# Kernel tuning notes

Hardware: AMD Instinct MI355X
Metric: run time of the kernel (lower is better)

The kernel has to match this reference:

```python
import jax, jax.numpy as jnp
import numpy as np

EPS = 1e-6
NH = 8     # num_head
WIN = 7    # window

def _ln(x, w, b):
    # channels_last LayerNorm over the final dim
    m = x.mean(-1, keepdims=True)
    v = ((x - m) ** 2).mean(-1, keepdims=True)
    return (x - m) / jnp.sqrt(v + EPS) * w + b

def _dwconv7(x, w, b):
    # x: (B, C, H, W); w: (C, 1, 7, 7) depthwise kernel; padding 3 (SAME for k=7)
    y = jax.lax.conv_general_dilated(
        x, w, window_strides=(1, 1), padding=((3, 3), (3, 3)),
        feature_group_count=x.shape[1],
        dimension_numbers=('NCHW', 'OIHW', 'NCHW'))
    return y + b[None, :, None, None]

def _forward(x, x_e, ln_w, ln_b, lne_w, lne_b, q_w, q_b, qcut_w, qcut_b,
             a_w, a_b, l_w, l_b, conv_w, conv_b, econv_w, econv_b,
             efore_w, efore_b, eback_w, eback_b, kv_w, kv_b,
             scl_w, scl_b, proj_w, proj_b, proje_w, proje_b):
    B, H, W, C = x.shape
    hd = C // NH // 2  # attention head dim (kv is split into k and v halves)

    xn = _ln(x, ln_w, ln_b)          # (B,H,W,C)
    xen = _ln(x_e, lne_w, lne_b)     # (B,H,W,C//2)

    # global shortcut branch (window != 0)
    short = jnp.concatenate([xn, xen], axis=3).transpose(0, 3, 1, 2)  # (B, 3C/2, H, W)

    q = xn @ q_w + q_b                # (B,H,W,C)
    cut = xn @ qcut_w + qcut_b        # (B,H,W,C//2)

    xl = jax.nn.gelu(xn @ l_w + l_b, approximate=False).transpose(0, 3, 1, 2)  # (B,C,H,W)
    a = _dwconv7(xl, conv_w, conv_b).transpose(0, 2, 3, 1) @ a_w + a_b          # (B,H,W,C)

    # kv from the activated l-branch (pre-conv)
    bfeat = xl.transpose(0, 2, 3, 1)                                  # (B,H,W,C)
    kv = (bfeat @ kv_w + kv_b).reshape(B, H * W, 2, NH, hd).transpose(2, 0, 3, 1, 4)
    k, v = kv[0], kv[1]                                               # (B,NH,HW,hd)

    # AdaptiveAvgPool2d((7,7)); H,W divisible by 7 -> exact uniform block mean
    pooled = short.reshape(B, -1, WIN, H // WIN, WIN, W // WIN).mean(axis=(3, 5))  # (B,3C/2,7,7)
    pooled = pooled.transpose(0, 2, 3, 1) @ scl_w + scl_b             # (B,7,7,C//2)
    m = pooled.reshape(B, WIN * WIN, NH, hd).transpose(0, 2, 1, 3)    # (B,NH,49,hd)

    attn = jax.nn.softmax((m * hd ** -0.5) @ jnp.swapaxes(k, -2, -1), axis=-1)  # (B,NH,49,HW)
    ao = (attn @ v).reshape(B, NH, WIN, WIN, hd).transpose(0, 1, 4, 2, 3).reshape(B, C // 2, WIN, WIN)
    ao = jax.image.resize(ao, (B, C // 2, H, W), method='bilinear').transpose(0, 2, 3, 1)  # (B,H,W,C//2)

    # depth branch: linear -> depthwise conv -> linear
    xe2 = (xen @ efore_w + efore_b).transpose(0, 3, 1, 2)             # (B,C//2,H,W)
    xe2 = _dwconv7(xe2, econv_w, econv_b).transpose(0, 2, 3, 1) @ eback_w + eback_b

    cut = cut * xe2
    xg = q * a
    cat = jnp.concatenate([xg, ao, cut], axis=3)                      # (B,H,W,2C)
    x_e_out = cat @ proje_w + proje_b                                 # (B,H,W,C//2)
    x_out = cat @ proj_w + proj_b                                     # (B,H,W,C)
    return x_out, x_e_out

def setup_inputs() -> dict:
    B, H, W, C = 16, 56, 84, 256
    key = jax.random.key(0)
    ks = jax.random.split(key, 16)
    def lin(k, din, dout):
        return jax.random.normal(k, (din, dout), jnp.float32) * float(1.0 / np.sqrt(din))
    return {
        'x': jax.random.normal(ks[0], (B, H, W, C), jnp.float32),
        'x_e': jax.random.normal(ks[1], (B, H, W, C // 2), jnp.float32),
        'ln_w': jnp.ones((C,), jnp.float32), 'ln_b': jnp.zeros((C,), jnp.float32),
        'lne_w': jnp.ones((C // 2,), jnp.float32), 'lne_b': jnp.zeros((C // 2,), jnp.float32),
        'q_w': lin(ks[2], C, C), 'q_b': jnp.zeros((C,), jnp.float32),
        'qcut_w': lin(ks[3], C, C // 2), 'qcut_b': jnp.zeros((C // 2,), jnp.float32),
        'a_w': lin(ks[4], C, C), 'a_b': jnp.zeros((C,), jnp.float32),
        'l_w': lin(ks[5], C, C), 'l_b': jnp.zeros((C,), jnp.float32),
        'conv_w': jax.random.normal(ks[6], (C, 1, 7, 7), jnp.float32) * 0.05,
        'conv_b': jnp.zeros((C,), jnp.float32),
        'econv_w': jax.random.normal(ks[7], (C // 2, 1, 7, 7), jnp.float32) * 0.05,
        'econv_b': jnp.zeros((C // 2,), jnp.float32),
        'efore_w': lin(ks[8], C // 2, C // 2), 'efore_b': jnp.zeros((C // 2,), jnp.float32),
        'eback_w': lin(ks[9], C // 2, C // 2), 'eback_b': jnp.zeros((C // 2,), jnp.float32),
        'kv_w': lin(ks[10], C, C), 'kv_b': jnp.zeros((C,), jnp.float32),
        'scl_w': lin(ks[11], C // 2 * 3, C // 2), 'scl_b': jnp.zeros((C // 2,), jnp.float32),
        'proj_w': lin(ks[12], 2 * C, C), 'proj_b': jnp.zeros((C,), jnp.float32),
        'proje_w': lin(ks[13], 2 * C, C // 2), 'proje_b': jnp.zeros((C // 2,), jnp.float32),
    }

def reference(x, x_e, ln_w, ln_b, lne_w, lne_b, q_w, q_b, qcut_w, qcut_b,
              a_w, a_b, l_w, l_b, conv_w, conv_b, econv_w, econv_b,
              efore_w, efore_b, eback_w, eback_b, kv_w, kv_b,
              scl_w, scl_b, proj_w, proj_b, proje_w, proje_b):
    return _forward(x, x_e, ln_w, ln_b, lne_w, lne_b, q_w, q_b, qcut_w, qcut_b,
                    a_w, a_b, l_w, l_b, conv_w, conv_b, econv_w, econv_b,
                    efore_w, efore_b, eback_w, eback_b, kv_w, kv_b,
                    scl_w, scl_b, proj_w, proj_b, proje_w, proje_b)
```

## Files before the change

kernel.cpp:

```cpp
#include <hip/hip_runtime.h>
#include <math.h>

#define N_TOK 75264
#define BDIM 16
#define HDIM 56
#define WDIM 84
#define CDIM 256
#define NHEAD 8
#define HWTOK 4704
#define NQ 49
#define SPLIT 8
#define TOKSPL 588
#define TSUB 84

typedef unsigned short u16;
typedef __attribute__((ext_vector_type(8))) short short8;
typedef __attribute__((ext_vector_type(4))) float floatx4;

__device__ __forceinline__ float bf2f(u16 u) {
    return __builtin_bit_cast(float, (unsigned)u << 16);
}
__device__ __forceinline__ u16 f2bf(float f) {
    unsigned u = __builtin_bit_cast(unsigned, f);
    u += 0x7fffu + ((u >> 16) & 1u);
    return (u16)(u >> 16);
}
__device__ __forceinline__ float gelu_exact(float v) {
    return 0.5f * v * (1.0f + erff(v * 0.70710678118654752f));
}

__global__ __launch_bounds__(256)
void wsplit_kernel(const float* __restrict__ q, const float* __restrict__ qcut,
                   const float* __restrict__ a, const float* __restrict__ l,
                   const float* __restrict__ kv, const float* __restrict__ efo,
                   const float* __restrict__ eba, const float* __restrict__ proj,
                   const float* __restrict__ proje,
                   u16* __restrict__ dh, u16* __restrict__ dl)
{
    int e = blockIdx.x * 256 + threadIdx.x;
    const float* src; int N, base, le;
    if (e < 65536)       { src = q;     N = 256; base = 0;      le = e; }
    else if (e < 98304)  { src = qcut;  N = 128; base = 65536;  le = e - 65536; }
    else if (e < 163840) { src = a;     N = 256; base = 98304;  le = e - 98304; }
    else if (e < 229376) { src = l;     N = 256; base = 163840; le = e - 163840; }
    else if (e < 294912) { src = kv;    N = 256; base = 229376; le = e - 229376; }
    else if (e < 311296) { src = efo;   N = 128; base = 294912; le = e - 294912; }
    else if (e < 327680) { src = eba;   N = 128; base = 311296; le = e - 311296; }
    else if (e < 458752) { src = proj;  N = 256; base = 327680; le = e - 327680; }
    else                 { src = proje; N = 128; base = 458752; le = e - 458752; }
    int K = (base >= 327680) ? 512 : ((base >= 294912) ? 128 : 256);
    int k = le / N, n = le & (N - 1);
    float w = src[le];
    u16 h = f2bf(w);
    dh[base + n * K + k] = h;
    dl[base + n * K + k] = f2bf(w - bf2f(h));
}

template<int CH>
__global__ __launch_bounds__(256)
void ln_kernel(const float* __restrict__ x, const float* __restrict__ w,
               const float* __restrict__ b, u16* __restrict__ oh, u16* __restrict__ ol)
{
    const int lane = threadIdx.x & 63;
    const int wv = threadIdx.x >> 6;
    const size_t tok = (size_t)blockIdx.x * 4 + wv;
    constexpr int V = CH / 64;
    float v[V];
    float s = 0.f, sq = 0.f;
    if constexpr (CH == 256) {
        float4 t4 = *(const float4*)(x + tok * CH + lane * 4);
        v[0] = t4.x; v[1] = t4.y; v[2] = t4.z; v[3] = t4.w;
    } else {
        float2 t2 = *(const float2*)(x + tok * CH + lane * 2);
        v[0] = t2.x; v[1] = t2.y;
    }
    #pragma unroll
    for (int i = 0; i < V; ++i) { s += v[i]; sq += v[i] * v[i]; }
    #pragma unroll
    for (int off = 32; off > 0; off >>= 1) {
        s += __shfl_xor(s, off);
        sq += __shfl_xor(sq, off);
    }
    const float mean = s * (1.0f / CH);
    const float var = sq * (1.0f / CH) - mean * mean;
    const float rstd = rsqrtf(var + 1e-6f);
    u16 hh[V], ll[V];
    #pragma unroll
    for (int i = 0; i < V; ++i) {
        float o = (v[i] - mean) * rstd * w[lane * V + i] + b[lane * V + i];
        hh[i] = f2bf(o);
        ll[i] = f2bf(o - bf2f(hh[i]));
    }
    if constexpr (CH == 256) {
        ushort4 th = {hh[0], hh[1], hh[2], hh[3]};
        ushort4 tl = {ll[0], ll[1], ll[2], ll[3]};
        *(ushort4*)(oh + tok * CH + lane * 4) = th;
        *(ushort4*)(ol + tok * CH + lane * 4) = tl;
    } else {
        ushort2 th = {hh[0], hh[1]};
        ushort2 tl = {ll[0], ll[1]};
        *(ushort2*)(oh + tok * CH + lane * 2) = th;
        *(ushort2*)(ol + tok * CH + lane * 2) = tl;
    }
}

__global__ __launch_bounds__(128)
void pool_scl_kernel(const u16* __restrict__ xnh, const u16* __restrict__ xnl,
                     const u16* __restrict__ xeh, const u16* __restrict__ xel,
                     const float* __restrict__ sclw, const float* __restrict__ sclb,
                     float* __restrict__ m)
{
    __shared__ float pooled[384];
    const int bp = blockIdx.x;
    const int b = bp / 49, p = bp % 49;
    const int py = p / 7, px = p % 7;
    const int tid = threadIdx.x;
    for (int ch = tid; ch < 384; ch += 128) {
        float acc = 0.f;
        for (int i = 0; i < 96; ++i) {
            int y = py * 8 + i / 12, x = px * 12 + i % 12;
            size_t pix = ((size_t)(b * HDIM + y) * WDIM + x);
            if (ch < 256) acc += bf2f(xnh[pix * 256 + ch]) + bf2f(xnl[pix * 256 + ch]);
            else          acc += bf2f(xeh[pix * 128 + ch - 256]) + bf2f(xel[pix * 128 + ch - 256]);
        }
        pooled[ch] = acc * (1.0f / 96.0f);
    }
    __syncthreads();
    float acc = sclb[tid];
    for (int k = 0; k < 384; ++k) acc = fmaf(pooled[k], sclw[k * 128 + tid], acc);
    m[(size_t)bp * 128 + tid] = acc;
}

#define BK 32
#define PADK 40
template<int EPI>
__global__ __launch_bounds__(256, 2)
void mgemm(const u16* __restrict__ Ah, const u16* __restrict__ Al, int lda,
           const u16* __restrict__ Bh, const u16* __restrict__ Bl, int K,
           const float* __restrict__ bias,
           u16* __restrict__ Dh, u16* __restrict__ Dl,
           float* __restrict__ Df, int ldd)
{
    __shared__ u16 AsH[128 * PADK], AsL[128 * PADK], BsH[128 * PADK], BsL[128 * PADK];
    const int t = threadIdx.x;
    const int m0 = blockIdx.x * 128, n0 = blockIdx.y * 128;
    const int sr = t >> 1;
    const int sk = (t & 1) * 16;
    const int lane = t & 63;
    const int w = t >> 6;
    const int wm = w >> 1, wn = w & 1;
    const int frow = lane & 15;
    const int fko = (lane >> 4) * 8;

    const u16* pAh = Ah + (size_t)(m0 + sr) * lda + sk;
    const u16* pAl = Al + (size_t)(m0 + sr) * lda + sk;
    const u16* pBh = Bh + (size_t)(n0 + sr) * K + sk;
    const u16* pBl = Bl + (size_t)(n0 + sr) * K + sk;

    int4 rAh0 = *(const int4*)(pAh);     int4 rAh1 = *(const int4*)(pAh + 8);
    int4 rAl0 = *(const int4*)(pAl);     int4 rAl1 = *(const int4*)(pAl + 8);
    int4 rBh0 = *(const int4*)(pBh);     int4 rBh1 = *(const int4*)(pBh + 8);
    int4 rBl0 = *(const int4*)(pBl);     int4 rBl1 = *(const int4*)(pBl + 8);

    floatx4 acc[4][4] = {};

    for (int k0 = 0; k0 < K; k0 += BK) {
        __syncthreads();
        *(int4*)&AsH[sr * PADK + sk] = rAh0;  *(int4*)&AsH[sr * PADK + sk + 8] = rAh1;
        *(int4*)&AsL[sr * PADK + sk] = rAl0;  *(int4*)&AsL[sr * PADK + sk + 8] = rAl1;
        *(int4*)&BsH[sr * PADK + sk] = rBh0;  *(int4*)&BsH[sr * PADK + sk + 8] = rBh1;
        *(int4*)&BsL[sr * PADK + sk] = rBl0;  *(int4*)&BsL[sr * PADK + sk + 8] = rBl1;
        __syncthreads();
        if (k0 + BK < K) {
            rAh0 = *(const int4*)(pAh + k0 + BK);  rAh1 = *(const int4*)(pAh + k0 + BK + 8);
            rAl0 = *(const int4*)(pAl + k0 + BK);  rAl1 = *(const int4*)(pAl + k0 + BK + 8);
            rBh0 = *(const int4*)(pBh + k0 + BK);  rBh1 = *(const int4*)(pBh + k0 + BK + 8);
            rBl0 = *(const int4*)(pBl + k0 + BK);  rBl1 = *(const int4*)(pBl + k0 + BK + 8);
        }
        short8 afh[4], afl[4], bfh[4], bfl[4];
        #pragma unroll
        for (int i = 0; i < 4; ++i) {
            int ar = wm * 64 + i * 16 + frow;
            afh[i] = *(const short8*)&AsH[ar * PADK + fko];
            afl[i] = *(const short8*)&AsL[ar * PADK + fko];
            int bc = wn * 64 + i * 16 + frow;
            bfh[i] = *(const short8*)&BsH[bc * PADK + fko];
            bfl[i] = *(const short8*)&BsL[bc * PADK + fko];
        }
        #pragma unroll
        for (int mt = 0; mt < 4; ++mt)
        #pragma unroll
        for (int nt = 0; nt < 4; ++nt) {
            acc[mt][nt] = __builtin_amdgcn_mfma_f32_16x16x32_bf16(afh[mt], bfh[nt], acc[mt][nt], 0, 0, 0);
            acc[mt][nt] = __builtin_amdgcn_mfma_f32_16x16x32_bf16(afh[mt], bfl[nt], acc[mt][nt], 0, 0, 0);
            acc[mt][nt] = __builtin_amdgcn_mfma_f32_16x16x32_bf16(afl[mt], bfh[nt], acc[mt][nt], 0, 0, 0);
        }
    }

    #pragma unroll
    for (int mt = 0; mt < 4; ++mt)
    #pragma unroll
    for (int nt = 0; nt < 4; ++nt)
    #pragma unroll
    for (int i = 0; i < 4; ++i) {
        int r = m0 + wm * 64 + mt * 16 + (lane >> 4) * 4 + i;
        int c = n0 + wn * 64 + nt * 16 + (lane & 15);
        float v = acc[mt][nt][i] + bias[c];
        size_t off = (size_t)r * ldd + c;
        if constexpr (EPI == 1) v = gelu_exact(v);
        if constexpr (EPI == 2) v *= bf2f(Dh[off]) + bf2f(Dl[off]);
        if constexpr (EPI == 3) {
            Df[off] = v;
        } else {
            u16 h = f2bf(v);
            Dh[off] = h;
            Dl[off] = f2bf(v - bf2f(h));
        }
    }
}

template<int C>
__global__ __launch_bounds__(256)
void dwconv7_kernel(const u16* __restrict__ inh, const u16* __restrict__ inl,
                    const float* __restrict__ w, const float* __restrict__ bias,
                    u16* __restrict__ outh, u16* __restrict__ outl)
{
    constexpr int QP = C / 4;
    constexpr int PPI = 256 / QP;
    constexpr int ITERS = 16 / PPI;
    __shared__ float wlds[49 * C];
    for (int idx = threadIdx.x; idx < C * 49; idx += 256) {
        int c = idx / 49, tap = idx % 49;
        wlds[tap * C + c] = w[idx];
    }
    __syncthreads();
    const int q = threadIdx.x % QP;
    const int sp = threadIdx.x / QP;
    const int c = q * 4;
    const int p0 = blockIdx.x * 16;
    float4 bv = *(const float4*)(bias + c);
    for (int it = 0; it < ITERS; ++it) {
        int p = p0 + it * PPI + sp;
        int x = p % WDIM;
        int tmp = p / WDIM;
        int y = tmp % HDIM;
        int b = tmp / HDIM;
        float4 acc = bv;
        for (int ky = 0; ky < 7; ++ky) {
            int yy = y + ky - 3;
            if (yy < 0 || yy >= HDIM) continue;
            const size_t rowoff = ((size_t)(b * HDIM + yy) * WDIM) * C;
            #pragma unroll
            for (int kx = 0; kx < 7; ++kx) {
                int xx = x + kx - 3;
                if (xx < 0 || xx >= WDIM) continue;
                ushort4 ih = *(const ushort4*)(inh + rowoff + (size_t)xx * C + c);
                ushort4 il = *(const ushort4*)(inl + rowoff + (size_t)xx * C + c);
                const float* wp = wlds + (ky * 7 + kx) * C + c;
                acc.x = fmaf(bf2f(ih.x) + bf2f(il.x), wp[0], acc.x);
                acc.y = fmaf(bf2f(ih.y) + bf2f(il.y), wp[1], acc.y);
                acc.z = fmaf(bf2f(ih.z) + bf2f(il.z), wp[2], acc.z);
                acc.w = fmaf(bf2f(ih.w) + bf2f(il.w), wp[3], acc.w);
            }
        }
        u16 h0 = f2bf(acc.x), h1 = f2bf(acc.y), h2 = f2bf(acc.z), h3 = f2bf(acc.w);
        ushort4 oh = {h0, h1, h2, h3};
        ushort4 ol = {f2bf(acc.x - bf2f(h0)), f2bf(acc.y - bf2f(h1)),
                      f2bf(acc.z - bf2f(h2)), f2bf(acc.w - bf2f(h3))};
        *(ushort4*)(outh + (size_t)p * C + c) = oh;
        *(ushort4*)(outl + (size_t)p * C + c) = ol;
    }
}

__global__ __launch_bounds__(256)
void attn_part_kernel(const float* __restrict__ m, const u16* __restrict__ kvh,
                      const u16* __restrict__ kvl,
                      float* __restrict__ Opart, float* __restrict__ mpart,
                      float* __restrict__ lpart)
{
    __shared__ float mq[NQ * 17];
    __shared__ float Ks[TSUB * 16];
    __shared__ float Vs[TSUB * 16];
    __shared__ float St[NQ * 85];
    __shared__ float Osm[NQ * 16];
    __shared__ float rowm[NQ], rowl[NQ], rowscale[NQ], rownewm[NQ];
    const int blk = blockIdx.x;
    const int bh = blk >> 3, s = blk & 7;
    const int b = bh >> 3, h = bh & 7;
    const int tid = threadIdx.x;
    const int tbase = s * TOKSPL;
    for (int i = tid; i < NQ * 16; i += 256) {
        int p = i >> 4, d = i & 15;
        mq[p * 17 + d] = m[((size_t)(b * 49 + p)) * 128 + h * 16 + d] * 0.25f;
        Osm[i] = 0.f;
    }
    if (tid < NQ) { rowm[tid] = -3.4e38f; rowl[tid] = 0.f; }
    __syncthreads();
    for (int c0 = 0; c0 < TOKSPL; c0 += TSUB) {
        const int t0 = tbase + c0;
        for (int i = tid; i < TSUB * 4; i += 256) {
            int row = i >> 2, q = (i & 3) << 2;
            size_t base = ((size_t)(b * HWTOK + t0 + row)) * 256 + h * 16 + q;
            ushort4 kh = *(const ushort4*)(kvh + base);
            ushort4 kl = *(const ushort4*)(kvl + base);
            ushort4 vh = *(const ushort4*)(kvh + base + 128);
            ushort4 vl = *(const ushort4*)(kvl + base + 128);
            Ks[row * 16 + q + 0] = bf2f(kh.x) + bf2f(kl.x);
            Ks[row * 16 + q + 1] = bf2f(kh.y) + bf2f(kl.y);
            Ks[row * 16 + q + 2] = bf2f(kh.z) + bf2f(kl.z);
            Ks[row * 16 + q + 3] = bf2f(kh.w) + bf2f(kl.w);
            Vs[row * 16 + q + 0] = bf2f(vh.x) + bf2f(vl.x);
            Vs[row * 16 + q + 1] = bf2f(vh.y) + bf2f(vl.y);
            Vs[row * 16 + q + 2] = bf2f(vh.z) + bf2f(vl.z);
            Vs[row * 16 + q + 3] = bf2f(vh.w) + bf2f(vl.w);
        }
        __syncthreads();
        for (int i = tid; i < NQ * TSUB; i += 256) {
            int p = i % NQ, t = i / NQ;
            const float* mp = &mq[p * 17];
            const float* kp = &Ks[t * 16];
            float sv = 0.f;
            #pragma unroll
            for (int d = 0; d < 16; ++d) sv = fmaf(mp[d], kp[d], sv);
            St[p * 85 + t] = sv;
        }
        __syncthreads();
        if (tid < NQ) {
            float mx = -3.4e38f;
            const float* sr = &St[tid * 85];
            for (int t = 0; t < TSUB; ++t) mx = fmaxf(mx, sr[t]);
            float nm = fmaxf(rowm[tid], mx);
            rownewm[tid] = nm;
            rowscale[tid] = expf(rowm[tid] - nm);
        }
        __syncthreads();
        for (int i = tid; i < NQ * TSUB; i += 256) {
            int p = i / TSUB, t = i % TSUB;
            St[p * 85 + t] = expf(St[p * 85 + t] - rownewm[p]);
        }
        __syncthreads();
        if (tid < NQ) {
            float sv = 0.f;
            const float* sr = &St[tid * 85];
            for (int t = 0; t < TSUB; ++t) sv += sr[t];
            rowl[tid] = rowl[tid] * rowscale[tid] + sv;
            rowm[tid] = rownewm[tid];
        }
        for (int i = tid; i < NQ * 16; i += 256) {
            int p = i >> 4, d = i & 15;
            float acc = Osm[i] * rowscale[p];
            const float* sr = &St[p * 85];
            const float* vp = &Vs[d];
            #pragma unroll 6
            for (int t = 0; t < TSUB; ++t) acc = fmaf(sr[t], vp[t * 16], acc);
            Osm[i] = acc;
        }
        __syncthreads();
    }
    for (int i = tid; i < NQ * 16; i += 256)
        Opart[(size_t)blk * (NQ * 16) + i] = Osm[i];
    if (tid < NQ) {
        mpart[blk * NQ + tid] = rowm[tid];
        lpart[blk * NQ + tid] = rowl[tid];
    }
}

__global__ __launch_bounds__(256)
void attn_combine_kernel(const float* __restrict__ Opart, const float* __restrict__ mpart,
                         const float* __restrict__ lpart, float* __restrict__ ao)
{
    const int bh = blockIdx.x;
    const int b = bh >> 3, h = bh & 7;
    const int tid = threadIdx.x;
    for (int i = tid; i < NQ * 16; i += 256) {
        int p = i >> 4, d = i & 15;
        float M = -3.4e38f;
        #pragma unroll
        for (int s = 0; s < SPLIT; ++s)
            M = fmaxf(M, mpart[(bh * SPLIT + s) * NQ + p]);
        float sO = 0.f, sl = 0.f;
        #pragma unroll
        for (int s = 0; s < SPLIT; ++s) {
            float e = expf(mpart[(bh * SPLIT + s) * NQ + p] - M);
            sl = fmaf(lpart[(bh * SPLIT + s) * NQ + p], e, sl);
            sO = fmaf(Opart[(size_t)(bh * SPLIT + s) * (NQ * 16) + i], e, sO);
        }
        ao[((size_t)(b * 49 + p)) * 128 + h * 16 + d] = sO / sl;
    }
}

__global__ __launch_bounds__(256)
void resize_kernel(const float* __restrict__ ao, u16* __restrict__ cath,
                   u16* __restrict__ catl)
{
    const int idx = blockIdx.x * 256 + threadIdx.x;
    const int c = idx & 127;
    const int p = idx >> 7;
    const int x = p % WDIM;
    int tmp = p / WDIM;
    const int y = tmp % HDIM;
    const int b = tmp / HDIM;
    float fy = (y + 0.5f) * 0.125f - 0.5f;
    float fx = (x + 0.5f) * (1.0f / 12.0f) - 0.5f;
    float yf = floorf(fy), xf = floorf(fx);
    int y0 = (int)yf, x0 = (int)xf;
    float wy = fy - yf, wx = fx - xf;
    int y1 = y0 + 1 < 6 ? y0 + 1 : 6;
    int x1 = x0 + 1 < 6 ? x0 + 1 : 6;
    y0 = y0 > 0 ? y0 : 0;
    x0 = x0 > 0 ? x0 : 0;
    const float* base = ao + (size_t)b * 49 * 128 + c;
    float v00 = base[(y0 * 7 + x0) * 128], v01 = base[(y0 * 7 + x1) * 128];
    float v10 = base[(y1 * 7 + x0) * 128], v11 = base[(y1 * 7 + x1) * 128];
    float r = (1.f - wy) * ((1.f - wx) * v00 + wx * v01)
            + wy * ((1.f - wx) * v10 + wx * v11);
    u16 h = f2bf(r);
    cath[(size_t)p * 512 + 256 + c] = h;
    catl[(size_t)p * 512 + 256 + c] = f2bf(r - bf2f(h));
}

extern "C" void kernel_launch(void* const* d_in, const int* in_sizes, int n_in,
                              void* d_out, int out_size, void* d_ws, size_t ws_size,
                              hipStream_t stream) {
    const float* x       = (const float*)d_in[0];
    const float* x_e     = (const float*)d_in[1];
    const float* ln_w    = (const float*)d_in[2];
    const float* ln_b    = (const float*)d_in[3];
    const float* lne_w   = (const float*)d_in[4];
    const float* lne_b   = (const float*)d_in[5];
    const float* q_w     = (const float*)d_in[6];
    const float* q_b     = (const float*)d_in[7];
    const float* qcut_w  = (const float*)d_in[8];
    const float* qcut_b  = (const float*)d_in[9];
    const float* a_w     = (const float*)d_in[10];
    const float* a_b     = (const float*)d_in[11];
    const float* l_w     = (const float*)d_in[12];
    const float* l_b     = (const float*)d_in[13];
    const float* conv_w  = (const float*)d_in[14];
    const float* conv_b  = (const float*)d_in[15];
    const float* econv_w = (const float*)d_in[16];
    const float* econv_b = (const float*)d_in[17];
    const float* efore_w = (const float*)d_in[18];
    const float* efore_b = (const float*)d_in[19];
    const float* eback_w = (const float*)d_in[20];
    const float* eback_b = (const float*)d_in[21];
    const float* kv_w    = (const float*)d_in[22];
    const float* kv_b    = (const float*)d_in[23];
    const float* scl_w   = (const float*)d_in[24];
    const float* scl_b   = (const float*)d_in[25];
    const float* proj_w  = (const float*)d_in[26];
    const float* proj_b  = (const float*)d_in[27];
    const float* proje_w = (const float*)d_in[28];
    const float* proje_b = (const float*)d_in[29];

    float* out_x = (float*)d_out;
    float* out_e = out_x + (size_t)N_TOK * 256;

    const size_t NT = N_TOK;

    u16* doutU = (u16*)d_out;
    u16* xlH  = doutU;
    u16* xlL  = xlH  + NT * 256;
    u16* xenH = xlL  + NT * 256;
    u16* xenL = xenH + NT * 128;

    u16* ws   = (u16*)d_ws;
    u16* xnH  = ws;
    u16* xnL  = xnH  + NT * 256;
    u16* catH = xnL  + NT * 256;
    u16* catL = catH + NT * 512;
    u16* wtH  = catL + NT * 512;
    u16* wtL  = wtH  + 524288;
    float* mbuf  = (float*)(wtL + 524288);
    float* aosm  = mbuf + 16 * 49 * 128;
    float* Opart = aosm + 16 * 49 * 128;
    float* mpart = Opart + 1024 * NQ * 16;
    float* lpart = mpart + 1024 * NQ;

    u16 *qtH = wtH + 0,      *qtL = wtL + 0;
    u16 *qctH = wtH + 65536, *qctL = wtL + 65536;
    u16 *atH = wtH + 98304,  *atL = wtL + 98304;
    u16 *ltH = wtH + 163840, *ltL = wtL + 163840;
    u16 *kvtH = wtH + 229376,*kvtL = wtL + 229376;
    u16 *efH = wtH + 294912, *efL = wtL + 294912;
    u16 *ebH = wtH + 311296, *ebL = wtL + 311296;
    u16 *pjH = wtH + 327680, *pjL = wtL + 327680;
    u16 *peH = wtH + 458752, *peL = wtL + 458752;

    u16 *cvH = xnH, *cvL = xnL;
    u16 *kvH = xnH, *kvL = xnL;
    u16 *e1H = xlH, *e1L = xlH + NT * 128;
    u16 *e2H = xlL, *e2L = xlL + NT * 128;

    dim3 g2(588, 2), g1(588, 1);

    wsplit_kernel<<<2048, 256, 0, stream>>>(q_w, qcut_w, a_w, l_w, kv_w, efore_w,
                                            eback_w, proj_w, proje_w, wtH, wtL);

    ln_kernel<256><<<N_TOK / 4, 256, 0, stream>>>(x, ln_w, ln_b, xnH, xnL);
    ln_kernel<128><<<N_TOK / 4, 256, 0, stream>>>(x_e, lne_w, lne_b, xenH, xenL);
    pool_scl_kernel<<<16 * 49, 128, 0, stream>>>(xnH, xnL, xenH, xenL, scl_w, scl_b, mbuf);

    mgemm<0><<<g2, 256, 0, stream>>>(xnH, xnL, 256, qtH, qtL, 256, q_b,
                                     catH, catL, nullptr, 512);
    mgemm<0><<<g1, 256, 0, stream>>>(xnH, xnL, 256, qctH, qctL, 256, qcut_b,
                                     catH + 384, catL + 384, nullptr, 512);
    mgemm<1><<<g2, 256, 0, stream>>>(xnH, xnL, 256, ltH, ltL, 256, l_b,
                                     xlH, xlL, nullptr, 256);
    dwconv7_kernel<256><<<N_TOK / 16, 256, 0, stream>>>(xlH, xlL, conv_w, conv_b, cvH, cvL);
    mgemm<2><<<g2, 256, 0, stream>>>(cvH, cvL, 256, atH, atL, 256, a_b,
                                     catH, catL, nullptr, 512);
    mgemm<0><<<g2, 256, 0, stream>>>(xlH, xlL, 256, kvtH, kvtL, 256, kv_b,
                                     kvH, kvL, nullptr, 256);
    attn_part_kernel<<<BDIM * NHEAD * SPLIT, 256, 0, stream>>>(mbuf, kvH, kvL,
                                                               Opart, mpart, lpart);
    attn_combine_kernel<<<BDIM * NHEAD, 256, 0, stream>>>(Opart, mpart, lpart, aosm);
    resize_kernel<<<(N_TOK * 128) / 256, 256, 0, stream>>>(aosm, catH, catL);

    mgemm<0><<<g1, 256, 0, stream>>>(xenH, xenL, 128, efH, efL, 128, efore_b,
                                     e1H, e1L, nullptr, 128);
    dwconv7_kernel<128><<<N_TOK / 16, 256, 0, stream>>>(e1H, e1L, econv_w, econv_b, e2H, e2L);
    mgemm<2><<<g1, 256, 0, stream>>>(e2H, e2L, 128, ebH, ebL, 128, eback_b,
                                     catH + 384, catL + 384, nullptr, 512);
    mgemm<3><<<g2, 256, 0, stream>>>(catH, catL, 512, pjH, pjL, 512, proj_b,
                                     nullptr, nullptr, out_x, 256);
    mgemm<3><<<g1, 256, 0, stream>>>(catH, catL, 512, peH, peL, 512, proje_b,
                                     nullptr, nullptr, out_e, 128);
}
```

Measured before the change: 1.613 ms.

## Pre-transpose depthwise conv weights once and drop per-block LDS staging

Depthwise conv weights are transposed to tap-major layout by a small one-off kernel instead of being reloaded and transposed into LDS by every conv block. The conv kernel is restructured so each thread handles 8 channels with 16-byte loads, one pixel per thread, reading weights straight from global memory (cached). This removes the per-block 49*C weight staging and barrier and widens loads, at the cost of more global/cache weight reads and more blocks.

```diff
diff --git a/kernel.cpp b/kernel.cpp
--- a/kernel.cpp
+++ b/kernel.cpp
@@ -15,6 +15,7 @@
 
 typedef unsigned short u16;
 typedef __attribute__((ext_vector_type(8))) short short8;
+typedef __attribute__((ext_vector_type(8))) unsigned short ushort8;
 typedef __attribute__((ext_vector_type(4))) float floatx4;
 
 __device__ __forceinline__ float bf2f(u16 u) {
@@ -56,6 +57,21 @@
     dl[base + n * K + k] = f2bf(w - bf2f(h));
 }
 
+__global__ __launch_bounds__(256)
+void cwt_kernel(const float* __restrict__ conv_w, const float* __restrict__ econv_w,
+                float* __restrict__ wt)
+{
+    int i = blockIdx.x * 256 + threadIdx.x;
+    if (i < 12544) {
+        int c = i / 49, tap = i % 49;
+        wt[tap * 256 + c] = conv_w[i];
+    } else if (i < 18816) {
+        int j = i - 12544;
+        int c = j / 49, tap = j % 49;
+        wt[12544 + tap * 128 + c] = econv_w[j];
+    }
+}
+
 template<int CH>
 __global__ __launch_bounds__(256)
 void ln_kernel(const float* __restrict__ x, const float* __restrict__ w,
@@ -222,54 +238,57 @@
 template<int C>
 __global__ __launch_bounds__(256)
 void dwconv7_kernel(const u16* __restrict__ inh, const u16* __restrict__ inl,
-                    const float* __restrict__ w, const float* __restrict__ bias,
+                    const float* __restrict__ wT, const float* __restrict__ bias,
                     u16* __restrict__ outh, u16* __restrict__ outl)
 {
-    constexpr int QP = C / 4;
-    constexpr int PPI = 256 / QP;
-    constexpr int ITERS = 16 / PPI;
-    __shared__ float wlds[49 * C];
-    for (int idx = threadIdx.x; idx < C * 49; idx += 256) {
-        int c = idx / 49, tap = idx % 49;
-        wlds[tap * C + c] = w[idx];
-    }
-    __syncthreads();
-    const int q = threadIdx.x % QP;
-    const int sp = threadIdx.x / QP;
-    const int c = q * 4;
-    const int p0 = blockIdx.x * 16;
-    float4 bv = *(const float4*)(bias + c);
-    for (int it = 0; it < ITERS; ++it) {
-        int p = p0 + it * PPI + sp;
-        int x = p % WDIM;
-        int tmp = p / WDIM;
-        int y = tmp % HDIM;
-        int b = tmp / HDIM;
-        float4 acc = bv;
-        for (int ky = 0; ky < 7; ++ky) {
-            int yy = y + ky - 3;
-            if (yy < 0 || yy >= HDIM) continue;
-            const size_t rowoff = ((size_t)(b * HDIM + yy) * WDIM) * C;
-            #pragma unroll
-            for (int kx = 0; kx < 7; ++kx) {
-                int xx = x + kx - 3;
-                if (xx < 0 || xx >= WDIM) continue;
-                ushort4 ih = *(const ushort4*)(inh + rowoff + (size_t)xx * C + c);
-                ushort4 il = *(const ushort4*)(inl + rowoff + (size_t)xx * C + c);
-                const float* wp = wlds + (ky * 7 + kx) * C + c;
-                acc.x = fmaf(bf2f(ih.x) + bf2f(il.x), wp[0], acc.x);
-                acc.y = fmaf(bf2f(ih.y) + bf2f(il.y), wp[1], acc.y);
-                acc.z = fmaf(bf2f(ih.z) + bf2f(il.z), wp[2], acc.z);
-                acc.w = fmaf(bf2f(ih.w) + bf2f(il.w), wp[3], acc.w);
-            }
-        }
-        u16 h0 = f2bf(acc.x), h1 = f2bf(acc.y), h2 = f2bf(acc.z), h3 = f2bf(acc.w);
-        ushort4 oh = {h0, h1, h2, h3};
-        ushort4 ol = {f2bf(acc.x - bf2f(h0)), f2bf(acc.y - bf2f(h1)),
-                      f2bf(acc.z - bf2f(h2)), f2bf(acc.w - bf2f(h3))};
-        *(ushort4*)(outh + (size_t)p * C + c) = oh;
-        *(ushort4*)(outl + (size_t)p * C + c) = ol;
-    }
+    constexpr int CPW = C / 8;
+    const int gid = blockIdx.x * 256 + threadIdx.x;
+    const int cw = gid & (CPW - 1);
+    const int p = gid / CPW;
+    const int c = cw * 8;
+    const int x = p % WDIM;
+    int tmp = p / WDIM;
+    const int y = tmp % HDIM;
+    const int b = tmp / HDIM;
+    float acc[8];
+    {
+        float4 b0 = *(const float4*)(bias + c);
+        float4 b1 = *(const float4*)(bias + c + 4);
+        acc[0] = b0.x; acc[1] = b0.y; acc[2] = b0.z; acc[3] = b0.w;
+        acc[4] = b1.x; acc[5] = b1.y; acc[6] = b1.z; acc[7] = b1.w;
+    }
+    for (int ky = 0; ky < 7; ++ky) {
+        int yy = y + ky - 3;
+        if (yy < 0 || yy >= HDIM) continue;
+        const size_t rowoff = ((size_t)(b * HDIM + yy) * WDIM) * C;
+        #pragma unroll
+        for (int kx = 0; kx < 7; ++kx) {
+            int xx = x + kx - 3;
+            if (xx < 0 || xx >= WDIM) continue;
+            ushort8 ih = *(const ushort8*)(inh + rowoff + (size_t)xx * C + c);
+            ushort8 il = *(const ushort8*)(inl + rowoff + (size_t)xx * C + c);
+            const float* wp = wT + (ky * 7 + kx) * C + c;
+            float4 w0 = *(const float4*)(wp);
+            float4 w1 = *(const float4*)(wp + 4);
+            acc[0] = fmaf(bf2f(ih[0]) + bf2f(il[0]), w0.x, acc[0]);
+            acc[1] = fmaf(bf2f(ih[1]) + bf2f(il[1]), w0.y, acc[1]);
+            acc[2] = fmaf(bf2f(ih[2]) + bf2f(il[2]), w0.z, acc[2]);
+            acc[3] = fmaf(bf2f(ih[3]) + bf2f(il[3]), w0.w, acc[3]);
+            acc[4] = fmaf(bf2f(ih[4]) + bf2f(il[4]), w1.x, acc[4]);
+            acc[5] = fmaf(bf2f(ih[5]) + bf2f(il[5]), w1.y, acc[5]);
+            acc[6] = fmaf(bf2f(ih[6]) + bf2f(il[6]), w1.z, acc[6]);
+            acc[7] = fmaf(bf2f(ih[7]) + bf2f(il[7]), w1.w, acc[7]);
+        }
+    }
+    ushort8 oh, ol;
+    #pragma unroll
+    for (int j = 0; j < 8; ++j) {
+        u16 h = f2bf(acc[j]);
+        oh[j] = h;
+        ol[j] = f2bf(acc[j] - bf2f(h));
+    }
+    *(ushort8*)(outh + (size_t)p * C + c) = oh;
+    *(ushort8*)(outl + (size_t)p * C + c) = ol;
 }
 
 __global__ __launch_bounds__(256)
@@ -476,6 +495,8 @@
     float* Opart = aosm + 16 * 49 * 128;
     float* mpart = Opart + 1024 * NQ * 16;
     float* lpart = mpart + 1024 * NQ;
+    float* cwT   = lpart + 1024 * NQ;
+    float* ecwT  = cwT + 12544;
 
     u16 *qtH = wtH + 0,      *qtL = wtL + 0;
     u16 *qctH = wtH + 65536, *qctL = wtL + 65536;
@@ -496,6 +517,7 @@
 
     wsplit_kernel<<<2048, 256, 0, stream>>>(q_w, qcut_w, a_w, l_w, kv_w, efore_w,
                                             eback_w, proj_w, proje_w, wtH, wtL);
+    cwt_kernel<<<74, 256, 0, stream>>>(conv_w, econv_w, cwT);
 
     ln_kernel<256><<<N_TOK / 4, 256, 0, stream>>>(x, ln_w, ln_b, xnH, xnL);
     ln_kernel<128><<<N_TOK / 4, 256, 0, stream>>>(x_e, lne_w, lne_b, xenH, xenL);
@@ -507,7 +529,7 @@
                                      catH + 384, catL + 384, nullptr, 512);
     mgemm<1><<<g2, 256, 0, stream>>>(xnH, xnL, 256, ltH, ltL, 256, l_b,
                                      xlH, xlL, nullptr, 256);
-    dwconv7_kernel<256><<<N_TOK / 16, 256, 0, stream>>>(xlH, xlL, conv_w, conv_b, cvH, cvL);
+    dwconv7_kernel<256><<<(N_TOK * 32) / 256, 256, 0, stream>>>(xlH, xlL, cwT, conv_b, cvH, cvL);
     mgemm<2><<<g2, 256, 0, stream>>>(cvH, cvL, 256, atH, atL, 256, a_b,
                                      catH, catL, nullptr, 512);
     mgemm<0><<<g2, 256, 0, stream>>>(xlH, xlL, 256, kvtH, kvtL, 256, kv_b,
@@ -519,7 +541,7 @@
 
     mgemm<0><<<g1, 256, 0, stream>>>(xenH, xenL, 128, efH, efL, 128, efore_b,
                                      e1H, e1L, nullptr, 128);
-    dwconv7_kernel<128><<<N_TOK / 16, 256, 0, stream>>>(e1H, e1L, econv_w, econv_b, e2H, e2L);
+    dwconv7_kernel<128><<<(N_TOK * 16) / 256, 256, 0, stream>>>(e1H, e1L, ecwT, econv_b, e2H, e2L);
     mgemm<2><<<g1, 256, 0, stream>>>(e2H, e2L, 128, ebH, ebL, 128, eback_b,
                                      catH + 384, catL + 384, nullptr, 512);
     mgemm<3><<<g2, 256, 0, stream>>>(catH, catL, 512, pjH, pjL, 512, proj_b,
```

Result: faster. 1.358 ms (-15.8%).
